# Optimization experiments

Hardware: AMD Instinct MI355X
Metric: run time of the kernel (lower is better)

Reference implementation:

```python
import jax, jax.numpy as jnp
import numpy as np

N = 100000
E = 1600000
EPS_BN = 1e-5
NEG_SLOPE = 0.2  # PyG GATConv default leaky_relu slope


def setup_inputs() -> dict:
    key = jax.random.key(0)
    ks = jax.random.split(key, 16)
    d = {}
    d['x'] = jax.random.normal(ks[0], (N, 128), jnp.float32)
    d['edge_index'] = jax.random.randint(ks[1], (2, E), 0, N, jnp.int64)
    d['W1'] = jax.random.normal(ks[2], (128, 128), jnp.float32) * 0.1
    d['att_src1'] = jax.random.normal(ks[3], (4, 32), jnp.float32) * 0.1
    d['att_dst1'] = jax.random.normal(ks[4], (4, 32), jnp.float32) * 0.1
    d['b1'] = jnp.zeros((128,), jnp.float32)
    d['bn1_gamma'] = jnp.ones((128,), jnp.float32)
    d['bn1_beta'] = jnp.zeros((128,), jnp.float32)
    d['bn1_mean'] = jnp.zeros((128,), jnp.float32)
    d['bn1_var'] = jax.random.uniform(ks[5], (128,), jnp.float32, 0.5, 1.5)
    d['W2'] = jax.random.normal(ks[6], (128, 64), jnp.float32) * 0.1
    d['att_src2'] = jax.random.normal(ks[7], (1, 64), jnp.float32) * 0.1
    d['att_dst2'] = jax.random.normal(ks[8], (1, 64), jnp.float32) * 0.1
    d['b2'] = jnp.zeros((64,), jnp.float32)
    d['bn2_gamma'] = jnp.ones((64,), jnp.float32)
    d['bn2_beta'] = jnp.zeros((64,), jnp.float32)
    d['bn2_mean'] = jnp.zeros((64,), jnp.float32)
    d['bn2_var'] = jax.random.uniform(ks[9], (64,), jnp.float32, 0.5, 1.5)
    return d


def _segment_softmax(e, dst, n):
    # numerically stable softmax over edges grouped by destination node
    m = jax.ops.segment_max(e, dst, num_segments=n)
    e = jnp.exp(e - m[dst])
    s = jax.ops.segment_sum(e, dst, num_segments=n)
    return e / s[dst]


def _gat_layer(x, src, dst, W, att_src, att_dst, b, heads, out_c, n):
    h = (x @ W).reshape(n, heads, out_c)            # [N,H,C]
    a_s = jnp.einsum('nhc,hc->nh', h, att_src)      # [N,H]
    a_d = jnp.einsum('nhc,hc->nh', h, att_dst)
    e = jax.nn.leaky_relu(a_s[src] + a_d[dst], NEG_SLOPE)  # [E,H]
    alpha = _segment_softmax(e, dst, n)
    out = jax.ops.segment_sum(alpha[:, :, None] * h[src], dst, num_segments=n)
    return out.reshape(n, heads * out_c) + b


def _bn_eval(x, gamma, beta, mean, var):
    return gamma * (x - mean) * jax.lax.rsqrt(var + EPS_BN) + beta


def reference(x, edge_index, W1, att_src1, att_dst1, b1, bn1_gamma, bn1_beta,
              bn1_mean, bn1_var, W2, att_src2, att_dst2, b2, bn2_gamma,
              bn2_beta, bn2_mean, bn2_var):
    n = x.shape[0]
    sl = jnp.arange(n, dtype=edge_index.dtype)      # PyG add_self_loops=True
    src = jnp.concatenate([edge_index[0], sl])
    dst = jnp.concatenate([edge_index[1], sl])
    # layer 1: GATConv(128 -> 32, heads=4, concat) + BN + ReLU (dropout=eval)
    h = _gat_layer(x, src, dst, W1, att_src1, att_dst1, b1, 4, 32, n)
    h = jax.nn.relu(_bn_eval(h, bn1_gamma, bn1_beta, bn1_mean, bn1_var))
    # layer 2: GATConv(128 -> 64, heads=1) + BN
    h = _gat_layer(h, src, dst, W2, att_src2, att_dst2, b2, 1, 64, n)
    return _bn_eval(h, bn2_gamma, bn2_beta, bn2_mean, bn2_var)
```

## Files before the change

### kernel.cpp

```cpp
#include <hip/hip_runtime.h>
#include <cstdint>
#include <cstddef>

#define NEG_SLOPE 0.2f
#define EPS_BN 1e-5f

__device__ __forceinline__ float leaky(float v) { return v > 0.f ? v : NEG_SLOPE * v; }

__device__ __forceinline__ unsigned short f2bf(float f) {
    unsigned u = __float_as_uint(f);
    u += 0x7fffu + ((u >> 16) & 1u);
    return (unsigned short)(u >> 16);
}
__device__ __forceinline__ float bf2f(unsigned short b) {
    return __uint_as_float(((unsigned)b) << 16);
}

__global__ __launch_bounds__(256) void gemm1_kernel(
    const float* __restrict__ x, const float* __restrict__ W,
    const float* __restrict__ att_src, const float* __restrict__ att_dst,
    unsigned short* __restrict__ hb, float* __restrict__ a_s, float* __restrict__ a_d,
    int n)
{
    __shared__ float Wl[128 * 128];
    __shared__ float xl[32 * 128];
    const int tid = threadIdx.x;
    const int c  = tid & 31;
    const int r4 = (tid >> 5) * 4;
    const int head = c >> 3;
    for (int i = tid; i < 128 * 128 / 4; i += 256)
        ((float4*)Wl)[i] = ((const float4*)W)[i];
    float atts[4], attd[4];
    #pragma unroll
    for (int j = 0; j < 4; ++j) {
        atts[j] = att_src[4 * c + j];
        attd[j] = att_dst[4 * c + j];
    }
    const int ntiles = n >> 5;
    for (int tile = blockIdx.x; tile < ntiles; tile += gridDim.x) {
        const int n0 = tile * 32;
        __syncthreads();
        for (int i = tid; i < 32 * 128 / 4; i += 256)
            ((float4*)xl)[i] = ((const float4*)(x + (size_t)n0 * 128))[i];
        __syncthreads();
        float acc[4][4];
        #pragma unroll
        for (int j = 0; j < 4; ++j)
            #pragma unroll
            for (int q = 0; q < 4; ++q) acc[j][q] = 0.f;
        #pragma unroll 4
        for (int k = 0; k < 128; k += 4) {
            float4 xv[4];
            #pragma unroll
            for (int q = 0; q < 4; ++q)
                xv[q] = *(const float4*)&xl[(r4 + q) * 128 + k];
            #pragma unroll
            for (int kk = 0; kk < 4; ++kk) {
                const float4 wv = *(const float4*)&Wl[(k + kk) * 128 + 4 * c];
                const float x0 = kk == 0 ? xv[0].x : kk == 1 ? xv[0].y : kk == 2 ? xv[0].z : xv[0].w;
                const float x1 = kk == 0 ? xv[1].x : kk == 1 ? xv[1].y : kk == 2 ? xv[1].z : xv[1].w;
                const float x2 = kk == 0 ? xv[2].x : kk == 1 ? xv[2].y : kk == 2 ? xv[2].z : xv[2].w;
                const float x3 = kk == 0 ? xv[3].x : kk == 1 ? xv[3].y : kk == 2 ? xv[3].z : xv[3].w;
                acc[0][0] += x0 * wv.x; acc[0][1] += x1 * wv.x; acc[0][2] += x2 * wv.x; acc[0][3] += x3 * wv.x;
                acc[1][0] += x0 * wv.y; acc[1][1] += x1 * wv.y; acc[1][2] += x2 * wv.y; acc[1][3] += x3 * wv.y;
                acc[2][0] += x0 * wv.z; acc[2][1] += x1 * wv.z; acc[2][2] += x2 * wv.z; acc[2][3] += x3 * wv.z;
                acc[3][0] += x0 * wv.w; acc[3][1] += x1 * wv.w; acc[3][2] += x2 * wv.w; acc[3][3] += x3 * wv.w;
            }
        }
        #pragma unroll
        for (int q = 0; q < 4; ++q) {
            const int row = n0 + r4 + q;
            ushort4 hv;
            hv.x = f2bf(acc[0][q]); hv.y = f2bf(acc[1][q]);
            hv.z = f2bf(acc[2][q]); hv.w = f2bf(acc[3][q]);
            *(ushort4*)(hb + (size_t)row * 128 + 4 * c) = hv;
            float vs = acc[0][q] * atts[0] + acc[1][q] * atts[1]
                     + acc[2][q] * atts[2] + acc[3][q] * atts[3];
            float vd = acc[0][q] * attd[0] + acc[1][q] * attd[1]
                     + acc[2][q] * attd[2] + acc[3][q] * attd[3];
            #pragma unroll
            for (int mm = 1; mm < 8; mm <<= 1) {
                vs += __shfl_xor(vs, mm);
                vd += __shfl_xor(vd, mm);
            }
            if ((c & 7) == 0) {
                a_s[row * 4 + head] = vs;
                a_d[row * 4 + head] = vd;
            }
        }
    }
}

__global__ __launch_bounds__(256) void gemm2_kernel(
    const float* __restrict__ x, const float* __restrict__ W,
    const float* __restrict__ att_src, const float* __restrict__ att_dst,
    unsigned short* __restrict__ hb, float* __restrict__ a_s, float* __restrict__ a_d,
    int n)
{
    __shared__ float Wl[128 * 64];
    __shared__ float xl[64 * 128];
    const int tid = threadIdx.x;
    const int c  = tid & 15;
    const int r4 = (tid >> 4) * 4;
    for (int i = tid; i < 128 * 64 / 4; i += 256)
        ((float4*)Wl)[i] = ((const float4*)W)[i];
    float atts[4], attd[4];
    #pragma unroll
    for (int j = 0; j < 4; ++j) {
        atts[j] = att_src[4 * c + j];
        attd[j] = att_dst[4 * c + j];
    }
    const int ntiles = (n + 63) >> 6;
    for (int tile = blockIdx.x; tile < ntiles; tile += gridDim.x) {
        const int n0 = tile * 64;
        __syncthreads();
        for (int i = tid; i < 64 * 128 / 4; i += 256) {
            const int row = n0 + (i >> 5);
            ((float4*)xl)[i] = (row < n) ? ((const float4*)(x + (size_t)n0 * 128))[i]
                                         : make_float4(0.f, 0.f, 0.f, 0.f);
        }
        __syncthreads();
        float acc[4][4];
        #pragma unroll
        for (int j = 0; j < 4; ++j)
            #pragma unroll
            for (int q = 0; q < 4; ++q) acc[j][q] = 0.f;
        #pragma unroll 4
        for (int k = 0; k < 128; k += 4) {
            float4 xv[4];
            #pragma unroll
            for (int q = 0; q < 4; ++q)
                xv[q] = *(const float4*)&xl[(r4 + q) * 128 + k];
            #pragma unroll
            for (int kk = 0; kk < 4; ++kk) {
                const float4 wv = *(const float4*)&Wl[(k + kk) * 64 + 4 * c];
                const float x0 = kk == 0 ? xv[0].x : kk == 1 ? xv[0].y : kk == 2 ? xv[0].z : xv[0].w;
                const float x1 = kk == 0 ? xv[1].x : kk == 1 ? xv[1].y : kk == 2 ? xv[1].z : xv[1].w;
                const float x2 = kk == 0 ? xv[2].x : kk == 1 ? xv[2].y : kk == 2 ? xv[2].z : xv[2].w;
                const float x3 = kk == 0 ? xv[3].x : kk == 1 ? xv[3].y : kk == 2 ? xv[3].z : xv[3].w;
                acc[0][0] += x0 * wv.x; acc[0][1] += x1 * wv.x; acc[0][2] += x2 * wv.x; acc[0][3] += x3 * wv.x;
                acc[1][0] += x0 * wv.y; acc[1][1] += x1 * wv.y; acc[1][2] += x2 * wv.y; acc[1][3] += x3 * wv.y;
                acc[2][0] += x0 * wv.z; acc[2][1] += x1 * wv.z; acc[2][2] += x2 * wv.z; acc[2][3] += x3 * wv.z;
                acc[3][0] += x0 * wv.w; acc[3][1] += x1 * wv.w; acc[3][2] += x2 * wv.w; acc[3][3] += x3 * wv.w;
            }
        }
        #pragma unroll
        for (int q = 0; q < 4; ++q) {
            const int row = n0 + r4 + q;
            float vs = acc[0][q] * atts[0] + acc[1][q] * atts[1]
                     + acc[2][q] * atts[2] + acc[3][q] * atts[3];
            float vd = acc[0][q] * attd[0] + acc[1][q] * attd[1]
                     + acc[2][q] * attd[2] + acc[3][q] * attd[3];
            if (row < n) {
                ushort4 hv;
                hv.x = f2bf(acc[0][q]); hv.y = f2bf(acc[1][q]);
                hv.z = f2bf(acc[2][q]); hv.w = f2bf(acc[3][q]);
                *(ushort4*)(hb + (size_t)row * 64 + 4 * c) = hv;
            }
            #pragma unroll
            for (int mm = 1; mm < 16; mm <<= 1) {
                vs += __shfl_xor(vs, mm);
                vd += __shfl_xor(vd, mm);
            }
            if (c == 0 && row < n) { a_s[row] = vs; a_d[row] = vd; }
        }
    }
}

__global__ __launch_bounds__(256) void hist_kernel(
    const int* __restrict__ ei, int* __restrict__ deg, int E, int NE)
{
    const int stride = gridDim.x * blockDim.x;
    for (int e = blockIdx.x * blockDim.x + threadIdx.x; e < NE; e += stride) {
        const int d = (e < E) ? ei[E + e] : e - E;
        atomicAdd(&deg[d], 1);
    }
}

__global__ __launch_bounds__(256) void scan1_kernel(
    const int* __restrict__ in, int* __restrict__ outp, int* __restrict__ bsums, int n)
{
    __shared__ int wsum[4];
    const int tid = threadIdx.x;
    const int lane = tid & 63, wid = tid >> 6;
    const int base = blockIdx.x * 1024 + tid * 4;
    int v0 = 0, v1 = 0, v2 = 0, v3 = 0;
    if (base + 0 < n) v0 = in[base + 0];
    if (base + 1 < n) v1 = in[base + 1];
    if (base + 2 < n) v2 = in[base + 2];
    if (base + 3 < n) v3 = in[base + 3];
    const int t = v0 + v1 + v2 + v3;
    int x = t;
    #pragma unroll
    for (int off = 1; off < 64; off <<= 1) {
        int y = __shfl_up(x, off);
        if (lane >= off) x += y;
    }
    if (lane == 63) wsum[wid] = x;
    __syncthreads();
    int woff = 0;
    #pragma unroll
    for (int w = 0; w < 4; ++w) if (w < wid) woff += wsum[w];
    const int excl = woff + x - t;
    if (base + 0 < n) outp[base + 0] = excl;
    if (base + 1 < n) outp[base + 1] = excl + v0;
    if (base + 2 < n) outp[base + 2] = excl + v0 + v1;
    if (base + 3 < n) outp[base + 3] = excl + v0 + v1 + v2;
    if (tid == 255) bsums[blockIdx.x] = woff + x;
}

__global__ __launch_bounds__(64) void scan2_kernel(int* bsums, int nb)
{
    const int lane = threadIdx.x;
    int carry = 0;
    for (int base = 0; base < nb; base += 64) {
        const int i = base + lane;
        const int v = (i < nb) ? bsums[i] : 0;
        int x = v;
        #pragma unroll
        for (int off = 1; off < 64; off <<= 1) {
            int y = __shfl_up(x, off);
            if (lane >= off) x += y;
        }
        if (i < nb) bsums[i] = carry + x - v;
        carry += __shfl(x, 63);
    }
}

__global__ __launch_bounds__(256) void scan3_kernel(
    const int* __restrict__ part, const int* __restrict__ bsums,
    int* __restrict__ rowptr, int* __restrict__ cur, int n, int ne)
{
    const int i = blockIdx.x * blockDim.x + threadIdx.x;
    if (i < n) {
        const int r = part[i] + bsums[i >> 10];
        rowptr[i] = r;
        cur[i] = r;
    }
    if (i == n) rowptr[n] = ne;
}

__global__ __launch_bounds__(256) void scatter_kernel(
    const int* __restrict__ ei, int* __restrict__ cur, int* __restrict__ csrc,
    int E, int NE)
{
    const int stride = gridDim.x * blockDim.x;
    for (int e = blockIdx.x * blockDim.x + threadIdx.x; e < NE; e += stride) {
        int s, d;
        if (e < E) { s = ei[e]; d = ei[E + e]; } else { s = d = e - E; }
        const int pos = atomicAdd(&cur[d], 1);
        csrc[pos] = s;
    }
}

__global__ __launch_bounds__(256) void agg1_csr_kernel(
    const int* __restrict__ rowptr, const int* __restrict__ csrc,
    const float* __restrict__ a_s, const float* __restrict__ a_d,
    const unsigned short* __restrict__ hb,
    const float* __restrict__ bias, const float* __restrict__ gamma,
    const float* __restrict__ beta, const float* __restrict__ mean,
    const float* __restrict__ var,
    float* __restrict__ outp, int n)
{
    const int lane = threadIdx.x & 63;
    const int wid = (blockIdx.x * blockDim.x + threadIdx.x) >> 6;
    const int nw = (gridDim.x * blockDim.x) >> 6;
    const int head = lane >> 4;
    const int dim0 = lane * 2;
    const float sc0 = gamma[dim0] * rsqrtf(var[dim0] + EPS_BN);
    const float of0 = sc0 * (bias[dim0] - mean[dim0]) + beta[dim0];
    const float sc1 = gamma[dim0 + 1] * rsqrtf(var[dim0 + 1] + EPS_BN);
    const float of1 = sc1 * (bias[dim0 + 1] - mean[dim0 + 1]) + beta[dim0 + 1];
    const unsigned* __restrict__ h32 = (const unsigned*)hb;

    const int chunk = (n + nw - 1) / nw;
    const int dlo = wid * chunk;
    const int dhi = min(n, dlo + chunk);
    for (int d = dlo; d < dhi; ++d) {
        const int b = rowptr[d], e = rowptr[d + 1];
        const float ad = a_d[d * 4 + head];
        float s0 = 0.f, s1 = 0.f, s2 = 0.f, s3 = 0.f;
        float x0 = 0.f, x1 = 0.f, x2 = 0.f, x3 = 0.f;
        float y0 = 0.f, y1 = 0.f, y2 = 0.f, y3 = 0.f;
        int i = b;
        for (; i + 4 <= e; i += 4) {
            const int nA = csrc[i], nB = csrc[i + 1], nC = csrc[i + 2], nD = csrc[i + 3];
            const float wA = __expf(leaky(a_s[nA * 4 + head] + ad));
            const float wB = __expf(leaky(a_s[nB * 4 + head] + ad));
            const float wC = __expf(leaky(a_s[nC * 4 + head] + ad));
            const float wD = __expf(leaky(a_s[nD * 4 + head] + ad));
            const unsigned uA = h32[(size_t)nA * 64 + lane];
            const unsigned uB = h32[(size_t)nB * 64 + lane];
            const unsigned uC = h32[(size_t)nC * 64 + lane];
            const unsigned uD = h32[(size_t)nD * 64 + lane];
            s0 += wA; x0 += wA * __uint_as_float(uA << 16); y0 += wA * __uint_as_float(uA & 0xffff0000u);
            s1 += wB; x1 += wB * __uint_as_float(uB << 16); y1 += wB * __uint_as_float(uB & 0xffff0000u);
            s2 += wC; x2 += wC * __uint_as_float(uC << 16); y2 += wC * __uint_as_float(uC & 0xffff0000u);
            s3 += wD; x3 += wD * __uint_as_float(uD << 16); y3 += wD * __uint_as_float(uD & 0xffff0000u);
        }
        for (; i < e; ++i) {
            const int nA = csrc[i];
            const float wA = __expf(leaky(a_s[nA * 4 + head] + ad));
            const unsigned uA = h32[(size_t)nA * 64 + lane];
            s0 += wA; x0 += wA * __uint_as_float(uA << 16); y0 += wA * __uint_as_float(uA & 0xffff0000u);
        }
        const float inv = 1.f / ((s0 + s1) + (s2 + s3));
        float2 o;
        o.x = fmaxf(sc0 * (((x0 + x1) + (x2 + x3)) * inv) + of0, 0.f);
        o.y = fmaxf(sc1 * (((y0 + y1) + (y2 + y3)) * inv) + of1, 0.f);
        *(float2*)(outp + (size_t)d * 128 + dim0) = o;
    }
}

__global__ __launch_bounds__(256) void agg2_csr_kernel(
    const int* __restrict__ rowptr, const int* __restrict__ csrc,
    const float* __restrict__ a_s, const float* __restrict__ a_d,
    const unsigned short* __restrict__ hb,
    const float* __restrict__ bias, const float* __restrict__ gamma,
    const float* __restrict__ beta, const float* __restrict__ mean,
    const float* __restrict__ var,
    float* __restrict__ outp, int n)
{
    const int lane = threadIdx.x & 63;
    const int wid = (blockIdx.x * blockDim.x + threadIdx.x) >> 6;
    const int nw = (gridDim.x * blockDim.x) >> 6;
    const float sc = gamma[lane] * rsqrtf(var[lane] + EPS_BN);
    const float of = sc * (bias[lane] - mean[lane]) + beta[lane];

    const int chunk = (n + nw - 1) / nw;
    const int dlo = wid * chunk;
    const int dhi = min(n, dlo + chunk);
    for (int d = dlo; d < dhi; ++d) {
        const int b = rowptr[d], e = rowptr[d + 1];
        const float ad = a_d[d];
        float s0 = 0.f, s1 = 0.f, s2 = 0.f, s3 = 0.f;
        float a0 = 0.f, a1 = 0.f, a2 = 0.f, a3 = 0.f;
        int i = b;
        for (; i + 4 <= e; i += 4) {
            const int nA = csrc[i], nB = csrc[i + 1], nC = csrc[i + 2], nD = csrc[i + 3];
            const float wA = __expf(leaky(a_s[nA] + ad));
            const float wB = __expf(leaky(a_s[nB] + ad));
            const float wC = __expf(leaky(a_s[nC] + ad));
            const float wD = __expf(leaky(a_s[nD] + ad));
            a0 += wA * bf2f(hb[(size_t)nA * 64 + lane]);
            a1 += wB * bf2f(hb[(size_t)nB * 64 + lane]);
            a2 += wC * bf2f(hb[(size_t)nC * 64 + lane]);
            a3 += wD * bf2f(hb[(size_t)nD * 64 + lane]);
            s0 += wA; s1 += wB; s2 += wC; s3 += wD;
        }
        for (; i < e; ++i) {
            const int nA = csrc[i];
            const float wA = __expf(leaky(a_s[nA] + ad));
            s0 += wA; a0 += wA * bf2f(hb[(size_t)nA * 64 + lane]);
        }
        outp[(size_t)d * 64 + lane] =
            sc * (((a0 + a1) + (a2 + a3)) / ((s0 + s1) + (s2 + s3))) + of;
    }
}

static inline size_t align256(size_t x) { return (x + 255) & ~(size_t)255; }

extern "C" void kernel_launch(void* const* d_in, const int* in_sizes, int n_in,
                              void* d_out, int out_size, void* d_ws, size_t ws_size,
                              hipStream_t stream) {
    const float* x        = (const float*)d_in[0];
    const int*   ei       = (const int*)d_in[1];
    const float* W1       = (const float*)d_in[2];
    const float* att_src1 = (const float*)d_in[3];
    const float* att_dst1 = (const float*)d_in[4];
    const float* b1       = (const float*)d_in[5];
    const float* bn1_g    = (const float*)d_in[6];
    const float* bn1_b    = (const float*)d_in[7];
    const float* bn1_m    = (const float*)d_in[8];
    const float* bn1_v    = (const float*)d_in[9];
    const float* W2       = (const float*)d_in[10];
    const float* att_src2 = (const float*)d_in[11];
    const float* att_dst2 = (const float*)d_in[12];
    const float* b2       = (const float*)d_in[13];
    const float* bn2_g    = (const float*)d_in[14];
    const float* bn2_b    = (const float*)d_in[15];
    const float* bn2_m    = (const float*)d_in[16];
    const float* bn2_v    = (const float*)d_in[17];

    const int N  = in_sizes[0] / 128;
    const int E  = in_sizes[1] / 2;
    const int NE = E + N;

    char* ws = (char*)d_ws;
    size_t off = 0;
    unsigned short* h1b = (unsigned short*)(ws + off); off = align256(off + (size_t)N * 128 * 2);
    unsigned short* h2b = (unsigned short*)(ws + off); off = align256(off + (size_t)N * 64 * 2);
    float* B      = (float*)(ws + off); off = align256(off + (size_t)N * 128 * 4);
    float* as1    = (float*)(ws + off); off = align256(off + (size_t)N * 4 * 4);
    float* ad1    = (float*)(ws + off); off = align256(off + (size_t)N * 4 * 4);
    float* as2    = (float*)(ws + off); off = align256(off + (size_t)N * 4);
    float* ad2    = (float*)(ws + off); off = align256(off + (size_t)N * 4);
    int* deg      = (int*)(ws + off);   off = align256(off + (size_t)N * 4);
    int* part     = (int*)(ws + off);   off = align256(off + (size_t)N * 4);
    int* rowptr   = (int*)(ws + off);   off = align256(off + (size_t)(N + 1) * 4);
    int* cur      = (int*)(ws + off);   off = align256(off + (size_t)N * 4);
    int* csrc     = (int*)(ws + off);   off = align256(off + (size_t)NE * 4);
    int* bsums    = (int*)(ws + off);   off = align256(off + 1024 * 4);
    float* out2   = (float*)d_out;

    const int nblocks_scan = (N + 1023) / 1024;

    hipMemsetAsync(deg, 0, (size_t)N * 4, stream);
    hist_kernel<<<2048, 256, 0, stream>>>(ei, deg, E, NE);
    scan1_kernel<<<nblocks_scan, 256, 0, stream>>>(deg, part, bsums, N);
    scan2_kernel<<<1, 64, 0, stream>>>(bsums, nblocks_scan);
    scan3_kernel<<<(N + 256) / 256, 256, 0, stream>>>(part, bsums, rowptr, cur, N, NE);
    scatter_kernel<<<2048, 256, 0, stream>>>(ei, cur, csrc, E, NE);

    gemm1_kernel<<<1024, 256, 0, stream>>>(x, W1, att_src1, att_dst1, h1b, as1, ad1, N);
    agg1_csr_kernel<<<2048, 256, 0, stream>>>(rowptr, csrc, as1, ad1, h1b,
                                              b1, bn1_g, bn1_b, bn1_m, bn1_v, B, N);

    gemm2_kernel<<<768, 256, 0, stream>>>(B, W2, att_src2, att_dst2, h2b, as2, ad2, N);
    agg2_csr_kernel<<<2048, 256, 0, stream>>>(rowptr, csrc, as2, ad2, h2b,
                                              b2, bn2_g, bn2_b, bn2_m, bn2_v, out2, N);
}
```

Before: 604.4 us.

## Build CSR via two-level bucket sort with shared-memory atomics

Replaces the global-atomic degree histogram, three-kernel scan and global-atomic scatter with a two-pass bucketed counting sort. Edges are first binned into 512-node buckets using per-block shared-memory counters and a single-block scan of the count matrix. Each bucket is then finalized into CSR in its own block using shared-memory atomics. This is meant to cut contended global atomics and random global writes, at the cost of an extra 8-byte-per-edge temporary pass and a serial single-block scan over K*256 counts.

```diff
diff --git a/kernel.cpp b/kernel.cpp
--- a/kernel.cpp
+++ b/kernel.cpp
@@ -4,6 +4,11 @@
 
 #define NEG_SLOPE 0.2f
 #define EPS_BN 1e-5f
+
+#define BKT_SHIFT 9
+#define BKT_SIZE 512
+#define MAXK 256
+#define PBLK 256
 
 __device__ __forceinline__ float leaky(float v) { return v > 0.f ? v : NEG_SLOPE * v; }
 
@@ -167,89 +172,114 @@
     }
 }
 
-__global__ __launch_bounds__(256) void hist_kernel(
-    const int* __restrict__ ei, int* __restrict__ deg, int E, int NE)
-{
-    const int stride = gridDim.x * blockDim.x;
-    for (int e = blockIdx.x * blockDim.x + threadIdx.x; e < NE; e += stride) {
+__global__ __launch_bounds__(256) void bucket_hist_kernel(
+    const int* __restrict__ ei, int* __restrict__ cnt_mat,
+    int E, int NE, int K, int CH)
+{
+    __shared__ int cnt[MAXK];
+    const int p = blockIdx.x;
+    for (int i = threadIdx.x; i < K; i += 256) cnt[i] = 0;
+    __syncthreads();
+    const int lo = p * CH, hi = min(NE, lo + CH);
+    for (int e = lo + threadIdx.x; e < hi; e += 256) {
         const int d = (e < E) ? ei[E + e] : e - E;
-        atomicAdd(&deg[d], 1);
-    }
-}
-
-__global__ __launch_bounds__(256) void scan1_kernel(
-    const int* __restrict__ in, int* __restrict__ outp, int* __restrict__ bsums, int n)
-{
-    __shared__ int wsum[4];
+        atomicAdd(&cnt[d >> BKT_SHIFT], 1);
+    }
+    __syncthreads();
+    for (int i = threadIdx.x; i < K; i += 256)
+        cnt_mat[i * PBLK + p] = cnt[i];
+}
+
+__global__ __launch_bounds__(1024) void scan_small_kernel(int* data, int M)
+{
+    __shared__ int wsums[16];
+    __shared__ int carry_s;
     const int tid = threadIdx.x;
-    const int lane = tid & 63, wid = tid >> 6;
-    const int base = blockIdx.x * 1024 + tid * 4;
-    int v0 = 0, v1 = 0, v2 = 0, v3 = 0;
-    if (base + 0 < n) v0 = in[base + 0];
-    if (base + 1 < n) v1 = in[base + 1];
-    if (base + 2 < n) v2 = in[base + 2];
-    if (base + 3 < n) v3 = in[base + 3];
-    const int t = v0 + v1 + v2 + v3;
+    const int lane = tid & 63, w = tid >> 6;
+    if (tid == 0) carry_s = 0;
+    __syncthreads();
+    for (int base = 0; base < M; base += 1024) {
+        const int i = base + tid;
+        const int v = (i < M) ? data[i] : 0;
+        int x = v;
+        #pragma unroll
+        for (int off = 1; off < 64; off <<= 1) {
+            int y = __shfl_up(x, off);
+            if (lane >= off) x += y;
+        }
+        if (lane == 63) wsums[w] = x;
+        __syncthreads();
+        int woff = 0;
+        #pragma unroll
+        for (int q = 0; q < 16; ++q) if (q < w) woff += wsums[q];
+        const int carry = carry_s;
+        __syncthreads();
+        if (i < M) data[i] = carry + woff + x - v;
+        if (tid == 1023) carry_s = carry + woff + x;
+        __syncthreads();
+    }
+}
+
+__global__ __launch_bounds__(256) void bucket_scatter_kernel(
+    const int* __restrict__ ei, const int* __restrict__ cnt_mat ,
+    uint2* __restrict__ tmp, int E, int NE, int K, int CH)
+{
+    __shared__ int offs[MAXK];
+    const int p = blockIdx.x;
+    for (int i = threadIdx.x; i < K; i += 256) offs[i] = cnt_mat[i * PBLK + p];
+    __syncthreads();
+    const int lo = p * CH, hi = min(NE, lo + CH);
+    for (int e = lo + threadIdx.x; e < hi; e += 256) {
+        int s, d;
+        if (e < E) { s = ei[e]; d = ei[E + e]; } else { s = d = e - E; }
+        const int pos = atomicAdd(&offs[d >> BKT_SHIFT], 1);
+        tmp[pos] = make_uint2((unsigned)s, (unsigned)d);
+    }
+}
+
+__global__ __launch_bounds__(256) void csr_finalize_kernel(
+    const uint2* __restrict__ tmp, const int* __restrict__ cnt_mat,
+    int* __restrict__ rowptr, int* __restrict__ csrc, int N, int NE, int K)
+{
+    __shared__ int cur[BKT_SIZE];
+    __shared__ int wsum2[4];
+    const int b = blockIdx.x;
+    const int base = b << BKT_SHIFT;
+    const int nn = min(BKT_SIZE, N - base);
+    const int elo = cnt_mat[b * PBLK];
+    const int ehi = (b + 1 < K) ? cnt_mat[(b + 1) * PBLK] : NE;
+    const int tid = threadIdx.x;
+    cur[tid] = 0; cur[tid + 256] = 0;
+    __syncthreads();
+    for (int i = elo + tid; i < ehi; i += 256)
+        atomicAdd(&cur[tmp[i].y - base], 1);
+    __syncthreads();
+    const int lane = tid & 63, w = tid >> 6;
+    const int v0 = cur[2 * tid], v1 = cur[2 * tid + 1];
+    const int t = v0 + v1;
     int x = t;
     #pragma unroll
     for (int off = 1; off < 64; off <<= 1) {
         int y = __shfl_up(x, off);
         if (lane >= off) x += y;
     }
-    if (lane == 63) wsum[wid] = x;
+    if (lane == 63) wsum2[w] = x;
     __syncthreads();
     int woff = 0;
     #pragma unroll
-    for (int w = 0; w < 4; ++w) if (w < wid) woff += wsum[w];
+    for (int q = 0; q < 4; ++q) if (q < w) woff += wsum2[q];
     const int excl = woff + x - t;
-    if (base + 0 < n) outp[base + 0] = excl;
-    if (base + 1 < n) outp[base + 1] = excl + v0;
-    if (base + 2 < n) outp[base + 2] = excl + v0 + v1;
-    if (base + 3 < n) outp[base + 3] = excl + v0 + v1 + v2;
-    if (tid == 255) bsums[blockIdx.x] = woff + x;
-}
-
-__global__ __launch_bounds__(64) void scan2_kernel(int* bsums, int nb)
-{
-    const int lane = threadIdx.x;
-    int carry = 0;
-    for (int base = 0; base < nb; base += 64) {
-        const int i = base + lane;
-        const int v = (i < nb) ? bsums[i] : 0;
-        int x = v;
-        #pragma unroll
-        for (int off = 1; off < 64; off <<= 1) {
-            int y = __shfl_up(x, off);
-            if (lane >= off) x += y;
-        }
-        if (i < nb) bsums[i] = carry + x - v;
-        carry += __shfl(x, 63);
-    }
-}
-
-__global__ __launch_bounds__(256) void scan3_kernel(
-    const int* __restrict__ part, const int* __restrict__ bsums,
-    int* __restrict__ rowptr, int* __restrict__ cur, int n, int ne)
-{
-    const int i = blockIdx.x * blockDim.x + threadIdx.x;
-    if (i < n) {
-        const int r = part[i] + bsums[i >> 10];
-        rowptr[i] = r;
-        cur[i] = r;
-    }
-    if (i == n) rowptr[n] = ne;
-}
-
-__global__ __launch_bounds__(256) void scatter_kernel(
-    const int* __restrict__ ei, int* __restrict__ cur, int* __restrict__ csrc,
-    int E, int NE)
-{
-    const int stride = gridDim.x * blockDim.x;
-    for (int e = blockIdx.x * blockDim.x + threadIdx.x; e < NE; e += stride) {
-        int s, d;
-        if (e < E) { s = ei[e]; d = ei[E + e]; } else { s = d = e - E; }
-        const int pos = atomicAdd(&cur[d], 1);
-        csrc[pos] = s;
+    __syncthreads();
+    cur[2 * tid] = excl;
+    cur[2 * tid + 1] = excl + v0;
+    if (2 * tid < nn)     rowptr[base + 2 * tid]     = elo + excl;
+    if (2 * tid + 1 < nn) rowptr[base + 2 * tid + 1] = elo + excl + v0;
+    if (b == K - 1 && tid == 0) rowptr[N] = NE;
+    __syncthreads();
+    for (int i = elo + tid; i < ehi; i += 256) {
+        const uint2 ed = tmp[i];
+        const int r = atomicAdd(&cur[ed.y - base], 1);
+        csrc[elo + r] = (int)ed.x;
     }
 }
 
@@ -385,6 +415,8 @@
     const int N  = in_sizes[0] / 128;
     const int E  = in_sizes[1] / 2;
     const int NE = E + N;
+    const int K  = (N + BKT_SIZE - 1) >> BKT_SHIFT;
+    const int CH = (NE + PBLK - 1) / PBLK;
 
     char* ws = (char*)d_ws;
     size_t off = 0;
@@ -395,22 +427,16 @@
     float* ad1    = (float*)(ws + off); off = align256(off + (size_t)N * 4 * 4);
     float* as2    = (float*)(ws + off); off = align256(off + (size_t)N * 4);
     float* ad2    = (float*)(ws + off); off = align256(off + (size_t)N * 4);
-    int* deg      = (int*)(ws + off);   off = align256(off + (size_t)N * 4);
-    int* part     = (int*)(ws + off);   off = align256(off + (size_t)N * 4);
     int* rowptr   = (int*)(ws + off);   off = align256(off + (size_t)(N + 1) * 4);
-    int* cur      = (int*)(ws + off);   off = align256(off + (size_t)N * 4);
     int* csrc     = (int*)(ws + off);   off = align256(off + (size_t)NE * 4);
-    int* bsums    = (int*)(ws + off);   off = align256(off + 1024 * 4);
+    uint2* tmp    = (uint2*)(ws + off); off = align256(off + (size_t)NE * 8);
+    int* cnt_mat  = (int*)(ws + off);   off = align256(off + (size_t)K * PBLK * 4);
     float* out2   = (float*)d_out;
 
-    const int nblocks_scan = (N + 1023) / 1024;
-
-    hipMemsetAsync(deg, 0, (size_t)N * 4, stream);
-    hist_kernel<<<2048, 256, 0, stream>>>(ei, deg, E, NE);
-    scan1_kernel<<<nblocks_scan, 256, 0, stream>>>(deg, part, bsums, N);
-    scan2_kernel<<<1, 64, 0, stream>>>(bsums, nblocks_scan);
-    scan3_kernel<<<(N + 256) / 256, 256, 0, stream>>>(part, bsums, rowptr, cur, N, NE);
-    scatter_kernel<<<2048, 256, 0, stream>>>(ei, cur, csrc, E, NE);
+    bucket_hist_kernel<<<PBLK, 256, 0, stream>>>(ei, cnt_mat, E, NE, K, CH);
+    scan_small_kernel<<<1, 1024, 0, stream>>>(cnt_mat, K * PBLK);
+    bucket_scatter_kernel<<<PBLK, 256, 0, stream>>>(ei, cnt_mat, tmp, E, NE, K, CH);
+    csr_finalize_kernel<<<K, 256, 0, stream>>>(tmp, cnt_mat, rowptr, csrc, N, NE, K);
 
     gemm1_kernel<<<1024, 256, 0, stream>>>(x, W1, att_src1, att_dst1, h1b, as1, ad1, N);
     agg1_csr_kernel<<<2048, 256, 0, stream>>>(rowptr, csrc, as1, ad1, h1b,
```

Result: faster. 491.3 us (-18.7%).
